# Optimization experiments

Measured on AMD Instinct MI355X. Metric: run time of the kernel, lower is better.

Reference implementation:

```python
import jax, jax.numpy as jnp
import numpy as np

# Static DAG configuration (mirrors GraphState): 1 input node + L layers of K nodes.
L = 8          # depth layers (well under t_budget=12)
K = 8          # nodes per layer
D = 128        # node hidden width (node.D)
B = 4096       # batch size
INDEG = 4      # in-edges per non-input node
N = 1 + L * K  # total nodes


def _build_graph():
    """Deterministic static edge lists: srcs[l][k, j] = parent node id (topologically earlier)."""
    rng = np.random.default_rng(0)
    srcs = []
    n_prev = 1  # node 0 is the INPUT node
    for _ in range(L):
        srcs.append(rng.integers(0, n_prev, size=(K, INDEG)))
        n_prev += K
    return srcs


def setup_inputs() -> dict:
    key = jax.random.key(0)
    k1, k2, k3 = jax.random.split(key, 3)
    X = jax.random.normal(k1, (B, D), dtype=jnp.float32)
    # scale ~ sqrt(2/(indeg*D)) to keep relu activations O(1) over 8 layers
    W = jax.random.normal(k2, (N, D, D), dtype=jnp.float32) * 0.06
    b = jax.random.normal(k3, (N, D), dtype=jnp.float32) * 0.01
    return {"X_batch": X, "W_all": W, "bias_all": b}


def reference(X_batch, W_all, bias_all):
    srcs = _build_graph()  # static python/numpy index constants -> jit-friendly
    # INPUT node (id 0): input_dim == D so no zero-padding; V_out = relu(X W^T + b)
    v0 = jax.nn.relu(X_batch @ W_all[0].T + bias_all[0])          # (B, D)
    outs = v0[None]                                               # (n_done, B, D)
    node = 1
    for l in range(L):
        idx = srcs[l]                                             # (K, INDEG) static
        V_in = outs[idx].sum(axis=1)                              # inbox gather-sum -> (K, B, D)
        Wl = W_all[node:node + K]                                 # (K, D, D)
        bl = bias_all[node:node + K]                              # (K, D)
        V_weighted = jnp.einsum('kbd,ked->kbe', V_in, Wl) + bl[:, None, :]
        V_out = jax.nn.relu(V_weighted)                           # apply_primitive(relu)
        outs = jnp.concatenate([outs, V_out], axis=0)
        node += K
    # output nodes = last layer; final = mean over fired output nodes
    return outs[-K:].mean(axis=0)                                 # (B, D)
```

## Files before the change

### kernel.cpp

```cpp
#include <hip/hip_runtime.h>
#include <cstdint>
#include <cstring>

#define BATCH   4096
#define DIM     128
#define NLAYERS 8
#define KNODES  8
#define NDEG    4
#define NNODES  65
#define NODE_ELEMS (BATCH * DIM)
#define ROWS    16
#define SLOTS   37
#define TILE_B  (ROWS * 256)
#define NTHREADS 1024

typedef float    f32x4 __attribute__((ext_vector_type(4)));
typedef short    s16x8 __attribute__((ext_vector_type(8)));
typedef uint32_t u32x4 __attribute__((ext_vector_type(4)));

struct LayerSrcs { int p[KNODES][NDEG]; };

struct Sched {
  uint64_t pinfo[NLAYERS * KNODES];
  int8_t   dst[NLAYERS * KNODES];
  int8_t   root_dst;
};

__device__ __forceinline__ uint32_t f2bf(float f) {
  union { float f; uint32_t i; } x; x.f = f;
  return (x.i + 0x7fffu + ((x.i >> 16) & 1u)) >> 16;
}
__device__ __forceinline__ uint32_t pack2(float a, float b) {
  return f2bf(a) | (f2bf(b) << 16);
}

__global__ __launch_bounds__(256)
void pack_w(const float* __restrict__ W, uint16_t* __restrict__ Wp) {
  int gid  = blockIdx.x * 256 + threadIdx.x;
  int lane = gid & 63;
  int n    = (gid >> 6) & 7;
  int ks   = (gid >> 9) & 3;
  int node = gid >> 11;
  int col  = n * 16 + (lane & 15);
  int k0   = ks * 32 + (lane >> 4) * 8;
  const float* src = W + ((size_t)node * DIM + col) * DIM + k0;
  f32x4 v0 = *(const f32x4*)src;
  f32x4 v1 = *(const f32x4*)(src + 4);
  u32x4 pk;
  pk.x = pack2(v0.x, v0.y); pk.y = pack2(v0.z, v0.w);
  pk.z = pack2(v1.x, v1.y); pk.w = pack2(v1.z, v1.w);
  *(u32x4*)(Wp + (size_t)gid * 8) = pk;
}

__global__ __launch_bounds__(NTHREADS, 4)
void dag_exec(const float* __restrict__ X, const uint16_t* __restrict__ Wp,
              const float* __restrict__ bias, uint16_t* __restrict__ outs,
              float* __restrict__ out, Sched sch)
{
  __shared__ char lds[SLOTS * TILE_B + 2048 * 4];
  float* mb = (float*)(lds + (size_t)SLOTS * TILE_B);

  const int t    = threadIdx.x;
  const int lane = t & 63;
  const int wv   = t >> 6;
  const int lr   = lane & 15;
  const int lg   = lane >> 4;
  const int kn   = wv & 7;
  const int h    = wv >> 3;
  const int row0 = blockIdx.x * ROWS;

  mb[t] = 0.f;
  mb[t + 1024] = 0.f;

  if (wv < 8) {
    f32x4 acc = (f32x4){0.f, 0.f, 0.f, 0.f};
    s16x8 wf[4];
#pragma unroll
    for (int ks = 0; ks < 4; ++ks)
      wf[ks] = *(const s16x8*)(Wp + (((size_t)(0 * 4 + ks) * 8 + wv) << 9) + lane * 8);
#pragma unroll
    for (int ks = 0; ks < 4; ++ks) {
      const float* xp = X + (size_t)(row0 + lr) * DIM + ks * 32 + lg * 8;
      f32x4 v0 = *(const f32x4*)xp;
      f32x4 v1 = *(const f32x4*)(xp + 4);
      u32x4 pk;
      pk.x = pack2(v0.x, v0.y); pk.y = pack2(v0.z, v0.w);
      pk.z = pack2(v1.x, v1.y); pk.w = pack2(v1.z, v1.w);
      s16x8 af;
      __builtin_memcpy(&af, &pk, 16);
      acc = __builtin_amdgcn_mfma_f32_16x16x32_bf16(af, wf[ks], acc, 0, 0, 0);
    }
    char* db = lds + (size_t)sch.root_dst * TILE_B;
    const int col = wv * 16 + lr;
    const float bv = bias[col];
#pragma unroll
    for (int j = 0; j < 4; ++j) {
      const int row = lg * 4 + j;
      float v = fmaxf(acc[j] + bv, 0.f);
      *(uint16_t*)(db + ((row * 256 + col * 2) ^ ((row & 7) << 4))) = (uint16_t)f2bf(v);
    }
  }
  __syncthreads();

  for (int l = 0; l < NLAYERS; ++l) {
    const int idx  = l * KNODES + kn;
    const int node = 1 + idx;
    const int dv   = sch.dst[idx];
    const uint64_t pinfo = sch.pinfo[idx];

    if (dv != -3) {
      const char* pbase[NDEG];
      bool pglob[NDEG];
#pragma unroll
      for (int p = 0; p < NDEG; ++p) {
        const int e  = (int)((pinfo >> (p * 16)) & 0xffff);
        const int ps = (e & 0xff) - 1;
        if (ps >= 0) {
          pbase[p] = lds + (size_t)ps * TILE_B;
          pglob[p] = false;
        } else {
          const int pid = e >> 8;
          pbase[p] = (const char*)(outs + (size_t)pid * NODE_ELEMS +
                                   (size_t)(row0 + lr) * DIM + lg * 8);
          pglob[p] = true;
        }
      }
      const uint16_t* wbase = Wp + ((((size_t)node * 4) * 8 + h * 4) << 9) + lane * 8;

      s16x8 wf[4][4];
      s16x8 af[4][4];

#pragma unroll
      for (int n = 0; n < 4; ++n)
        wf[0][n] = *(const s16x8*)(wbase + (size_t)(0 * 8 + n) * 512);
#pragma unroll
      for (int n = 0; n < 4; ++n)
        wf[1][n] = *(const s16x8*)(wbase + (size_t)(1 * 8 + n) * 512);
#pragma unroll
      for (int p = 0; p < NDEG; ++p)
        af[0][p] = pglob[p]
          ? *(const s16x8*)(pbase[p] + 0 * 64)
          : *(const s16x8*)(pbase[p] + ((lr * 256 + 0 * 64 + lg * 16) ^ ((lr & 7) << 4)));
      float bv[4];
#pragma unroll
      for (int n = 0; n < 4; ++n)
        bv[n] = bias[(size_t)node * DIM + (h * 4 + n) * 16 + lr];

      f32x4 acc[4];
#pragma unroll
      for (int n = 0; n < 4; ++n) acc[n] = (f32x4){0.f, 0.f, 0.f, 0.f};

#pragma unroll
      for (int ks = 0; ks < 4; ++ks) {
        if (ks + 2 < 4) {
#pragma unroll
          for (int n = 0; n < 4; ++n)
            wf[ks + 2][n] = *(const s16x8*)(wbase + (size_t)((ks + 2) * 8 + n) * 512);
        }
        if (ks + 1 < 4) {
#pragma unroll
          for (int p = 0; p < NDEG; ++p)
            af[ks + 1][p] = pglob[p]
              ? *(const s16x8*)(pbase[p] + (ks + 1) * 64)
              : *(const s16x8*)(pbase[p] +
                  ((lr * 256 + (ks + 1) * 64 + lg * 16) ^ ((lr & 7) << 4)));
        }
#pragma unroll
        for (int n = 0; n < 4; ++n)
#pragma unroll
          for (int p = 0; p < NDEG; ++p)
            acc[n] = __builtin_amdgcn_mfma_f32_16x16x32_bf16(af[ks][p], wf[ks][n], acc[n], 0, 0, 0);
      }

#pragma unroll
      for (int n = 0; n < 4; ++n) {
        const int col = (h * 4 + n) * 16 + lr;
        if (dv >= 0) {
          char* db = lds + (size_t)dv * TILE_B;
#pragma unroll
          for (int j = 0; j < 4; ++j) {
            const int row = lg * 4 + j;
            float v = fmaxf(acc[n][j] + bv[n], 0.f);
            *(uint16_t*)(db + ((row * 256 + col * 2) ^ ((row & 7) << 4))) = (uint16_t)f2bf(v);
          }
        } else if (dv == -1) {
          uint16_t* gb = outs + (size_t)node * NODE_ELEMS + (size_t)row0 * DIM + col;
#pragma unroll
          for (int j = 0; j < 4; ++j) {
            const int row = lg * 4 + j;
            float v = fmaxf(acc[n][j] + bv[n], 0.f);
            gb[(size_t)row * DIM] = (uint16_t)f2bf(v);
          }
        } else {
#pragma unroll
          for (int j = 0; j < 4; ++j) {
            const int row = lg * 4 + j;
            float v = fmaxf(acc[n][j] + bv[n], 0.f);
            atomicAdd(mb + row * DIM + col, v);
          }
        }
      }
    }
    __syncthreads();
  }

  {
    const int r = t >> 7, c = t & 127;
    out[(size_t)(row0 + r) * DIM + c]     = mb[t] * 0.125f;
    out[(size_t)(row0 + 8 + r) * DIM + c] = mb[t + 1024] * 0.125f;
  }
}

namespace nprng {
static inline uint32_t hashmix(uint32_t v, uint32_t& hc) {
  v ^= hc; hc *= 0x931e8875u; v *= hc; v ^= v >> 16; return v;
}
static inline uint32_t mixf(uint32_t x, uint32_t y) {
  uint32_t r = x * 0xca01f9ddu - y * 0x4973f715u;
  r ^= r >> 16;
  return r;
}
struct Pcg {
  unsigned __int128 state, inc;
  bool has32; uint32_t saved;
  void step() {
    const unsigned __int128 MUL =
        ((unsigned __int128)2549297995355413924ULL << 64) | 4865540595714422341ULL;
    state = state * MUL + inc;
  }
  void init_seed0() {
    uint32_t pool[4];
    uint32_t hc = 0x43b0d7e5u;
    for (int i = 0; i < 4; ++i) pool[i] = hashmix(0u, hc);
    for (int s = 0; s < 4; ++s)
      for (int d = 0; d < 4; ++d)
        if (s != d) pool[d] = mixf(pool[d], hashmix(pool[s], hc));
    uint32_t st[8];
    uint32_t hb = 0x8b51f9ddu;
    int cyc = 0;
    for (int i = 0; i < 8; ++i) {
      uint32_t dv = pool[cyc]; cyc = (cyc + 1) & 3;
      dv ^= hb; hb *= 0x58f38dedu; dv *= hb; dv ^= dv >> 16;
      st[i] = dv;
    }
    uint64_t v[4];
    for (int i = 0; i < 4; ++i)
      v[i] = (uint64_t)st[2 * i] | ((uint64_t)st[2 * i + 1] << 32);
    unsigned __int128 s128 = ((unsigned __int128)v[0] << 64) | v[1];
    unsigned __int128 i128 = ((unsigned __int128)v[2] << 64) | v[3];
    state = 0; inc = (i128 << 1) | 1;
    step(); state += s128; step();
    has32 = false; saved = 0;
  }
  uint64_t next64() {
    step();
    uint64_t rot = (uint64_t)(state >> 122);
    uint64_t x = (uint64_t)(state >> 64) ^ (uint64_t)state;
    return rot ? ((x >> rot) | (x << (64 - rot))) : x;
  }
  uint32_t next32() {
    if (has32) { has32 = false; return saved; }
    uint64_t v = next64();
    has32 = true; saved = (uint32_t)(v >> 32);
    return (uint32_t)v;
  }
  uint32_t lemire32(uint32_t rng_incl) {
    uint32_t rng_excl = rng_incl + 1u;
    uint64_t m = (uint64_t)next32() * (uint64_t)rng_excl;
    uint32_t leftover = (uint32_t)m;
    if (leftover < rng_excl) {
      uint32_t threshold = (0xFFFFFFFFu - rng_incl) % rng_excl;
      while (leftover < threshold) {
        m = (uint64_t)next32() * (uint64_t)rng_excl;
        leftover = (uint32_t)m;
      }
    }
    return (uint32_t)(m >> 32);
  }
};
}

extern "C" void kernel_launch(void* const* d_in, const int* in_sizes, int n_in,
                              void* d_out, int out_size, void* d_ws, size_t ws_size,
                              hipStream_t stream) {
  const float* X    = (const float*)d_in[0];
  const float* W    = (const float*)d_in[1];
  const float* bias = (const float*)d_in[2];
  float* out        = (float*)d_out;

  uint16_t* Wp   = (uint16_t*)d_ws;
  uint16_t* outs = (uint16_t*)((char*)d_ws + (size_t)NNODES * DIM * DIM * 2);

  nprng::Pcg rng; rng.init_seed0();
  LayerSrcs srcs[NLAYERS];
  int n_prev = 1;
  for (int l = 0; l < NLAYERS; ++l) {
    for (int k = 0; k < KNODES; ++k)
      for (int j = 0; j < NDEG; ++j)
        srcs[l].p[k][j] = (n_prev == 1) ? 0 : (int)rng.lemire32((uint32_t)(n_prev - 1));
    n_prev += KNODES;
  }

  bool alive[NNODES];
  for (int i = 0; i < NNODES; ++i) alive[i] = false;
  for (int i = NNODES - KNODES; i < NNODES; ++i) alive[i] = true;
  for (int l = NLAYERS - 1; l >= 0; --l)
    for (int k = 0; k < KNODES; ++k)
      if (alive[1 + l * KNODES + k])
        for (int j = 0; j < NDEG; ++j) alive[srcs[l].p[k][j]] = true;

  int last_use[NNODES];
  for (int i = 0; i < NNODES; ++i) last_use[i] = -1;
  for (int l = 0; l < NLAYERS; ++l)
    for (int k = 0; k < KNODES; ++k)
      if (alive[1 + l * KNODES + k])
        for (int j = 0; j < NDEG; ++j) {
          int s = srcs[l].p[k][j];
          if (l > last_use[s]) last_use[s] = l;
        }

  int slot_of[NNODES];
  for (int i = 0; i < NNODES; ++i) slot_of[i] = -1;
  int freeStk[SLOTS], nfree = 0;
  for (int i = SLOTS - 1; i >= 0; --i) freeStk[nfree++] = i;

  Sched sch;
  slot_of[0] = freeStk[--nfree];
  sch.root_dst = (int8_t)slot_of[0];

  for (int l = 0; l < NLAYERS; ++l) {
    for (int k = 0; k < KNODES; ++k) {
      const int node = 1 + l * KNODES + k;
      int dv;
      if (!alive[node])            dv = -3;
      else if (l == NLAYERS - 1)   dv = -2;
      else if (nfree > 0)          dv = slot_of[node] = freeStk[--nfree];
      else                         dv = -1;
      sch.dst[l * KNODES + k] = (int8_t)dv;

      uint64_t w64 = 0;
      for (int j = 0; j < NDEG; ++j) {
        const int src = srcs[l].p[k][j];
        const int enc = ((slot_of[src] + 1) & 0xff) | (src << 8);
        w64 |= (uint64_t)enc << (j * 16);
      }
      sch.pinfo[l * KNODES + k] = w64;
    }
    for (int n = 0; n < NNODES; ++n)
      if (slot_of[n] >= 0 && last_use[n] == l) {
        freeStk[nfree++] = slot_of[n];
        slot_of[n] = -1;
      }
  }

  pack_w<<<dim3(520), dim3(256), 0, stream>>>(W, Wp);
  dag_exec<<<dim3(BATCH / ROWS), dim3(NTHREADS), 0, stream>>>(X, Wp, bias, outs, out, sch);
}
```

Measured before the change: 123.0 us.

## Prefetch next layer's weights across barriers and use LDS-only barriers

Weight fragments for the whole K loop are now double-buffered in registers, and the next layer's weights are loaded right after the current layer's MFMAs, so global-memory latency overlaps the epilogue and the barrier. The per-layer __syncthreads is replaced by an lgkmcnt-only wait plus s_barrier unless that layer spills to global memory, which avoids waiting on outstanding vector-memory loads. The MFMA section also raises wave priority. This costs 64 extra VGPRs for the second weight buffer, which could raise register pressure at 1024 threads per block.

```diff
diff --git a/kernel.cpp b/kernel.cpp
--- a/kernel.cpp
+++ b/kernel.cpp
@@ -24,6 +24,7 @@
   uint64_t pinfo[NLAYERS * KNODES];
   int8_t   dst[NLAYERS * KNODES];
   int8_t   root_dst;
+  uint32_t spillmask;
 };
 
 __device__ __forceinline__ uint32_t f2bf(float f) {
@@ -32,6 +33,9 @@
 }
 __device__ __forceinline__ uint32_t pack2(float a, float b) {
   return f2bf(a) | (f2bf(b) << 16);
+}
+__device__ __forceinline__ void barrier_lgkm() {
+  asm volatile("s_waitcnt lgkmcnt(0)\n\ts_barrier" ::: "memory");
 }
 
 __global__ __launch_bounds__(256)
@@ -72,12 +76,22 @@
   mb[t] = 0.f;
   mb[t + 1024] = 0.f;
 
+  s16x8 wf[2][4][4];
+
+#define PREFETCH_WF(buf, node_) do {                                          \
+    const uint16_t* wb_ = Wp + ((((size_t)(node_) * 4) * 8 + h * 4) << 9)     \
+                          + lane * 8;                                         \
+    _Pragma("unroll") for (int ks_ = 0; ks_ < 4; ++ks_)                       \
+    _Pragma("unroll") for (int n_ = 0; n_ < 4; ++n_)                          \
+      wf[buf][ks_][n_] = *(const s16x8*)(wb_ + (size_t)(ks_ * 8 + n_) * 512); \
+  } while (0)
+
   if (wv < 8) {
     f32x4 acc = (f32x4){0.f, 0.f, 0.f, 0.f};
-    s16x8 wf[4];
+    s16x8 rwf[4];
 #pragma unroll
     for (int ks = 0; ks < 4; ++ks)
-      wf[ks] = *(const s16x8*)(Wp + (((size_t)(0 * 4 + ks) * 8 + wv) << 9) + lane * 8);
+      rwf[ks] = *(const s16x8*)(Wp + (((size_t)ks * 8 + wv) << 9) + lane * 8);
 #pragma unroll
     for (int ks = 0; ks < 4; ++ks) {
       const float* xp = X + (size_t)(row0 + lr) * DIM + ks * 32 + lg * 8;
@@ -88,7 +102,7 @@
       pk.z = pack2(v1.x, v1.y); pk.w = pack2(v1.z, v1.w);
       s16x8 af;
       __builtin_memcpy(&af, &pk, 16);
-      acc = __builtin_amdgcn_mfma_f32_16x16x32_bf16(af, wf[ks], acc, 0, 0, 0);
+      acc = __builtin_amdgcn_mfma_f32_16x16x32_bf16(af, rwf[ks], acc, 0, 0, 0);
     }
     char* db = lds + (size_t)sch.root_dst * TILE_B;
     const int col = wv * 16 + lr;
@@ -100,9 +114,12 @@
       *(uint16_t*)(db + ((row * 256 + col * 2) ^ ((row & 7) << 4))) = (uint16_t)f2bf(v);
     }
   }
-  __syncthreads();
-
+  PREFETCH_WF(0, 1 + kn);
+  barrier_lgkm();
+
+#pragma unroll
   for (int l = 0; l < NLAYERS; ++l) {
+    const int cur  = l & 1;
     const int idx  = l * KNODES + kn;
     const int node = 1 + idx;
     const int dv   = sch.dst[idx];
@@ -125,52 +142,45 @@
           pglob[p] = true;
         }
       }
-      const uint16_t* wbase = Wp + ((((size_t)node * 4) * 8 + h * 4) << 9) + lane * 8;
-
-      s16x8 wf[4][4];
-      s16x8 af[4][4];
-
+      float bv[4];
 #pragma unroll
       for (int n = 0; n < 4; ++n)
-        wf[0][n] = *(const s16x8*)(wbase + (size_t)(0 * 8 + n) * 512);
-#pragma unroll
-      for (int n = 0; n < 4; ++n)
-        wf[1][n] = *(const s16x8*)(wbase + (size_t)(1 * 8 + n) * 512);
+        bv[n] = bias[(size_t)node * DIM + (h * 4 + n) * 16 + lr];
+
+      f32x4 acc[4];
+#pragma unroll
+      for (int n = 0; n < 4; ++n) acc[n] = (f32x4){0.f, 0.f, 0.f, 0.f};
+
+      s16x8 afA[NDEG], afB[NDEG];
 #pragma unroll
       for (int p = 0; p < NDEG; ++p)
-        af[0][p] = pglob[p]
+        afA[p] = pglob[p]
           ? *(const s16x8*)(pbase[p] + 0 * 64)
           : *(const s16x8*)(pbase[p] + ((lr * 256 + 0 * 64 + lg * 16) ^ ((lr & 7) << 4)));
-      float bv[4];
-#pragma unroll
-      for (int n = 0; n < 4; ++n)
-        bv[n] = bias[(size_t)node * DIM + (h * 4 + n) * 16 + lr];
-
-      f32x4 acc[4];
-#pragma unroll
-      for (int n = 0; n < 4; ++n) acc[n] = (f32x4){0.f, 0.f, 0.f, 0.f};
-
+
+      __builtin_amdgcn_s_setprio(1);
 #pragma unroll
       for (int ks = 0; ks < 4; ++ks) {
-        if (ks + 2 < 4) {
-#pragma unroll
-          for (int n = 0; n < 4; ++n)
-            wf[ks + 2][n] = *(const s16x8*)(wbase + (size_t)((ks + 2) * 8 + n) * 512);
-        }
         if (ks + 1 < 4) {
 #pragma unroll
-          for (int p = 0; p < NDEG; ++p)
-            af[ks + 1][p] = pglob[p]
+          for (int p = 0; p < NDEG; ++p) {
+            s16x8 v = pglob[p]
               ? *(const s16x8*)(pbase[p] + (ks + 1) * 64)
               : *(const s16x8*)(pbase[p] +
                   ((lr * 256 + (ks + 1) * 64 + lg * 16) ^ ((lr & 7) << 4)));
+            if (ks & 1) afA[p] = v; else afB[p] = v;
+          }
         }
 #pragma unroll
         for (int n = 0; n < 4; ++n)
 #pragma unroll
           for (int p = 0; p < NDEG; ++p)
-            acc[n] = __builtin_amdgcn_mfma_f32_16x16x32_bf16(af[ks][p], wf[ks][n], acc[n], 0, 0, 0);
-      }
+            acc[n] = __builtin_amdgcn_mfma_f32_16x16x32_bf16(
+                (ks & 1) ? afB[p] : afA[p], wf[cur][ks][n], acc[n], 0, 0, 0);
+      }
+      __builtin_amdgcn_s_setprio(0);
+
+      if (l + 1 < NLAYERS) PREFETCH_WF(cur ^ 1, 1 + (l + 1) * KNODES + kn);
 
 #pragma unroll
       for (int n = 0; n < 4; ++n) {
@@ -200,8 +210,12 @@
           }
         }
       }
-    }
-    __syncthreads();
+    } else {
+      if (l + 1 < NLAYERS) PREFETCH_WF(cur ^ 1, 1 + (l + 1) * KNODES + kn);
+    }
+
+    if (sch.spillmask & (1u << l)) __syncthreads();
+    else                           barrier_lgkm();
   }
 
   {
@@ -209,6 +223,7 @@
     out[(size_t)(row0 + r) * DIM + c]     = mb[t] * 0.125f;
     out[(size_t)(row0 + 8 + r) * DIM + c] = mb[t + 1024] * 0.125f;
   }
+#undef PREFETCH_WF
 }
 
 namespace nprng {
@@ -325,6 +340,7 @@
   for (int i = SLOTS - 1; i >= 0; --i) freeStk[nfree++] = i;
 
   Sched sch;
+  sch.spillmask = 0;
   slot_of[0] = freeStk[--nfree];
   sch.root_dst = (int8_t)slot_of[0];
 
@@ -335,7 +351,7 @@
       if (!alive[node])            dv = -3;
       else if (l == NLAYERS - 1)   dv = -2;
       else if (nfree > 0)          dv = slot_of[node] = freeStk[--nfree];
-      else                         dv = -1;
+      else                         { dv = -1; sch.spillmask |= (1u << l); }
       sch.dst[l * KNODES + k] = (int8_t)dv;
 
       uint64_t w64 = 0;
```

Measured after the change: 154.6 us. +25.7%, slower.
